# Kernel optimization log

Measured on AMD Instinct MI355X. Metric: run time of the kernel, lower is better.

Reference implementation:

```python
import jax, jax.numpy as jnp
import numpy as np

BATCH, SEQ = 4, 2048
D_MODEL, D_STATE, D_CONV, HEADDIM = 512, 128, 4, 64
D_INNER = 1024          # expand * d_model
NHEADS = 16             # d_inner / headdim
CONV_DIM = D_INNER + 2 * D_STATE   # 1280 (ngroups=1)
D_IN_PROJ = 2 * D_INNER + 2 * D_STATE + NHEADS  # 2320


def setup_inputs() -> dict:
    key = jax.random.key(0)
    ks = jax.random.split(key, 7)
    x = jax.random.normal(ks[0], (BATCH, SEQ, D_MODEL), jnp.float32)
    norm_weight = jnp.ones((D_MODEL,), jnp.float32)
    in_proj_w = jax.random.normal(ks[1], (D_IN_PROJ, D_MODEL), jnp.float32) * 0.02
    conv_w = jax.random.normal(ks[2], (CONV_DIM, 1, D_CONV), jnp.float32) * 0.2
    conv_b = jnp.zeros((CONV_DIM,), jnp.float32)
    dt_bias = jax.random.normal(ks[3], (NHEADS,), jnp.float32) * 0.1
    A_log = jnp.log(jax.random.uniform(ks[4], (NHEADS,), jnp.float32, 1.0, 16.0))
    D_param = jnp.ones((NHEADS,), jnp.float32)
    gated_norm_weight = jnp.ones((D_INNER,), jnp.float32)
    out_proj_w = jax.random.normal(ks[5], (D_MODEL, D_INNER), jnp.float32) * 0.02
    return dict(x=x, norm_weight=norm_weight, in_proj_w=in_proj_w, conv_w=conv_w,
                conv_b=conv_b, dt_bias=dt_bias, A_log=A_log, D_param=D_param,
                gated_norm_weight=gated_norm_weight, out_proj_w=out_proj_w)


def _rmsnorm(x, w, eps):
    return w * (x * jax.lax.rsqrt(jnp.mean(x * x, axis=-1, keepdims=True) + eps))


def _mamba2_forward(x, norm_weight, in_proj_w, conv_w, conv_b, dt_bias,
                    A_log, D_param, gated_norm_weight, out_proj_w):
    b, l, _ = x.shape
    u = _rmsnorm(x, norm_weight, 1e-6)                       # pre-norm (eps=1e-6)
    zxbcdt = u @ in_proj_w.T                                 # (b,l,2320)
    z = zxbcdt[..., :D_INNER]                                # gate
    xBC = zxbcdt[..., D_INNER:D_INNER + CONV_DIM]            # (b,l,1280)
    dt = zxbcdt[..., D_INNER + CONV_DIM:]                    # (b,l,nheads)
    dt = jax.nn.softplus(dt + dt_bias)

    # causal depthwise conv1d over time + SiLU
    conv = jax.lax.conv_general_dilated(
        xBC.transpose(0, 2, 1), conv_w, window_strides=(1,),
        padding=[(D_CONV - 1, 0)], feature_group_count=CONV_DIM,
        dimension_numbers=('NCH', 'OIH', 'NCH'))
    xBC = jax.nn.silu((conv + conv_b[None, :, None]).transpose(0, 2, 1))

    xs = xBC[..., :D_INNER].reshape(b, l, NHEADS, HEADDIM)   # (b,l,h,p)
    Bmat = xBC[..., D_INNER:D_INNER + D_STATE]               # (b,l,n)
    Cmat = xBC[..., D_INNER + D_STATE:]                      # (b,l,n)

    A = -jnp.exp(A_log)                                      # (h,)
    dA = jnp.exp(dt * A)                                     # (b,l,h)
    dtx = dt[..., None] * xs                                 # (b,l,h,p)

    def step(h, inp):
        dA_t, dtx_t, B_t, C_t = inp                          # (b,h),(b,h,p),(b,n),(b,n)
        h = h * dA_t[..., None, None] + dtx_t[..., None] * B_t[:, None, None, :]
        y = jnp.einsum('bhpn,bn->bhp', h, C_t)
        return h, y

    h0 = jnp.zeros((b, NHEADS, HEADDIM, D_STATE), x.dtype)
    _, ys = jax.lax.scan(step, h0, (dA.transpose(1, 0, 2), dtx.transpose(1, 0, 2, 3),
                                    Bmat.transpose(1, 0, 2), Cmat.transpose(1, 0, 2)))
    y = ys.transpose(1, 0, 2, 3) + xs * D_param[None, None, :, None]  # D skip
    y = y.reshape(b, l, D_INNER)

    y = _rmsnorm(y * jax.nn.silu(z), gated_norm_weight, 1e-5)  # RMSNormGated (eps=1e-5)
    return x + y @ out_proj_w.T                                # residual


def reference(x, norm_weight, in_proj_w, conv_w, conv_b, dt_bias,
              A_log, D_param, gated_norm_weight, out_proj_w):
    return _mamba2_forward(x, norm_weight, in_proj_w, conv_w, conv_b, dt_bias,
                           A_log, D_param, gated_norm_weight, out_proj_w)
```

## Files before the change

### kernel.cpp

```cpp
#include <hip/hip_runtime.h>
#include <cstdint>
#include <cstddef>

#define B_ 4
#define L_ 2048
#define DMODEL 512
#define DINNER 1024
#define DSTATE 128
#define NH 16
#define HD 64
#define CONVDIM 1280
#define NPROJ 2320
#define NPAD 2432
#define ML (B_*L_)
#define Q_ 64
#define NCH 32

typedef __bf16 bf16x8 __attribute__((ext_vector_type(8)));
typedef float f32x4 __attribute__((ext_vector_type(4)));
typedef float f32x16 __attribute__((ext_vector_type(16)));

__device__ __forceinline__ float bf2f(ushort u) {
  union { unsigned int i; float f; } v; v.i = ((unsigned int)u) << 16; return v.f;
}
__device__ __forceinline__ ushort f2bf(float f) {
  union { float f; unsigned int i; } v; v.f = f;
  unsigned int u = v.i;
  unsigned int r = (u + 0x7fffu + ((u >> 16) & 1u)) >> 16;
  return (ushort)r;
}
__device__ __forceinline__ float siluf(float x) { return x / (1.f + __expf(-x)); }

__device__ __forceinline__ void gl_lds16(const void* g, void* l) {
  __builtin_amdgcn_global_load_lds(
      (const __attribute__((address_space(1))) unsigned int*)g,
      (__attribute__((address_space(3))) unsigned int*)l,
      16, 0, 0);
}

__global__ __launch_bounds__(256) void k_cvt(const float* __restrict__ wi, const float* __restrict__ wo,
                                             const float* __restrict__ gw,
                                             ushort* __restrict__ oi, ushort* __restrict__ oo) {
  int idx = blockIdx.x * 256 + threadIdx.x;
  const int n1 = NPAD * DMODEL;
  if (idx < n1) {
    int n = idx / DMODEL, k = idx % DMODEL;
    oi[idx] = f2bf((n < NPROJ) ? wi[(size_t)n * DMODEL + k] : 0.f);
  } else {
    int j = idx - n1;
    if (j < DMODEL * DINNER) oo[j] = f2bf(wo[j] * gw[j & (DINNER - 1)]);
  }
}

__global__ __launch_bounds__(256) void k_rmsnorm(const float* __restrict__ x, const float* __restrict__ w,
                                                 ushort* __restrict__ u) {
  int row = blockIdx.x * 4 + (threadIdx.x >> 6);
  int lane = threadIdx.x & 63;
  const float* xr = x + (size_t)row * DMODEL + lane * 8;
  float4 a = *(const float4*)xr;
  float4 b = *(const float4*)(xr + 4);
  float ss = a.x*a.x + a.y*a.y + a.z*a.z + a.w*a.w + b.x*b.x + b.y*b.y + b.z*b.z + b.w*b.w;
  ss += __shfl_xor(ss, 1);  ss += __shfl_xor(ss, 2);  ss += __shfl_xor(ss, 4);
  ss += __shfl_xor(ss, 8);  ss += __shfl_xor(ss, 16); ss += __shfl_xor(ss, 32);
  float sc = rsqrtf(ss * (1.f / DMODEL) + 1e-6f);
  const float* wr = w + lane * 8;
  float4 wa = *(const float4*)wr;
  float4 wb = *(const float4*)(wr + 4);
  union { ushort s[8]; int4 v; } o;
  o.s[0] = f2bf(a.x * wa.x * sc); o.s[1] = f2bf(a.y * wa.y * sc);
  o.s[2] = f2bf(a.z * wa.z * sc); o.s[3] = f2bf(a.w * wa.w * sc);
  o.s[4] = f2bf(b.x * wb.x * sc); o.s[5] = f2bf(b.y * wb.y * sc);
  o.s[6] = f2bf(b.z * wb.z * sc); o.s[7] = f2bf(b.w * wb.w * sc);
  *(int4*)(u + (size_t)row * DMODEL + lane * 8) = o.v;
}

template <int EPI, int BM, int BN, int MR, int NR>
__global__ __launch_bounds__(256) void gemm_bt(const ushort* __restrict__ A, const ushort* __restrict__ Bm,
                                               void* __restrict__ Cout, const float* __restrict__ resid,
                                               const float* __restrict__ rescale,
                                               int M, int N, int K, int gx) {
  constexpr int WM = MR * 32, WN = NR * 32;
  constexpr int WAVES_N = BN / WN;
  constexpr int CH_A = BM / 8, CH_B = BN / 8;
  constexpr int PER_A = CH_A / 4, PER_B = CH_B / 4;
  constexpr int SL = PER_A + PER_B;
  __shared__ __align__(16) ushort lA[2][BM * 64];
  __shared__ __align__(16) ushort lB[2][BN * 64];
  const int nwg = gridDim.x;
  const int cpx = nwg >> 3;
  const int bid = blockIdx.x;
  const int swz = (bid & 7) * cpx + (bid >> 3);
  const int n0 = (swz % gx) * BN, m0 = (swz / gx) * BM;
  const int t = threadIdx.x;
  const int wave = t >> 6, lane = t & 63;
  const int wr = wave / WAVES_N, wc = wave % WAVES_N;
  const int r3 = lane >> 3;
  const int ce = (((lane & 7) ^ r3) << 3);
  const int nt = K >> 6;
  f32x16 acc[MR][NR] = {};
  auto stage = [&](int buf, int k0) {
#pragma unroll
    for (int i = 0; i < PER_A; ++i) {
      int chunk = wave * PER_A + i;
      int row = chunk * 8 + r3;
      gl_lds16(A + (size_t)(m0 + row) * K + k0 + ce, (char*)&lA[buf][0] + chunk * 1024);
    }
#pragma unroll
    for (int i = 0; i < PER_B; ++i) {
      int chunk = wave * PER_B + i;
      int row = chunk * 8 + r3;
      gl_lds16(Bm + (size_t)(n0 + row) * K + k0 + ce, (char*)&lB[buf][0] + chunk * 1024);
    }
  };
  stage(0, 0);
  const int rsel = lane & 31;
  const int khi = (lane >> 5) << 3;
  const int kswz = (lane & 7) << 3;
  for (int kt = 0; kt < nt; ++kt) {
    const int cur = kt & 1;
    if (kt + 1 < nt) {
      stage(cur ^ 1, (kt + 1) << 6);
      if constexpr (SL == 8) asm volatile("s_waitcnt vmcnt(8)" ::: "memory");
      else if constexpr (SL == 6) asm volatile("s_waitcnt vmcnt(6)" ::: "memory");
      else asm volatile("s_waitcnt vmcnt(0)" ::: "memory");
    } else {
      asm volatile("s_waitcnt vmcnt(0)" ::: "memory");
    }
    __builtin_amdgcn_s_barrier();
#pragma unroll
    for (int kk = 0; kk < 64; kk += 16) {
      const int kcol = (kk + khi) ^ kswz;
      bf16x8 af[MR], bfr[NR];
#pragma unroll
      for (int m = 0; m < MR; ++m)
        af[m] = *reinterpret_cast<const bf16x8*>(&lA[cur][(wr * WM + m * 32 + rsel) * 64 + kcol]);
#pragma unroll
      for (int n = 0; n < NR; ++n)
        bfr[n] = *reinterpret_cast<const bf16x8*>(&lB[cur][(wc * WN + n * 32 + rsel) * 64 + kcol]);
#pragma unroll
      for (int m = 0; m < MR; ++m)
#pragma unroll
        for (int n = 0; n < NR; ++n)
          acc[m][n] = __builtin_amdgcn_mfma_f32_32x32x16_bf16(af[m], bfr[n], acc[m][n], 0, 0, 0);
    }
    __builtin_amdgcn_s_barrier();
  }
  const int coln = lane & 31;
  const int rbase = (lane >> 5) << 2;
#pragma unroll
  for (int m = 0; m < MR; ++m) {
#pragma unroll
    for (int n = 0; n < NR; ++n) {
      int gm0 = m0 + wr * WM + m * 32 + rbase;
      int gn = n0 + wc * WN + n * 32 + coln;
#pragma unroll
      for (int r = 0; r < 16; ++r) {
        int gm = gm0 + (r & 3) + 8 * (r >> 2);
        float v = acc[m][n][r];
        if (EPI == 0) {
          ((ushort*)Cout)[(size_t)gm * N + gn] = f2bf(v);
        } else {
          ((float*)Cout)[(size_t)gm * N + gn] = v * rescale[gm] + resid[(size_t)gm * N + gn];
        }
      }
    }
  }
}

__global__ __launch_bounds__(256) void k_dtcum(const ushort* __restrict__ zx, const float* __restrict__ dt_bias,
                                               const float* __restrict__ A_log, float* __restrict__ dtb,
                                               float* __restrict__ acum, float* __restrict__ rs) {
  int flat = blockIdx.x * 256 + threadIdx.x;
  if (flat < ML) rs[flat] = 0.f;
  int gid = blockIdx.x * 4 + (threadIdx.x >> 6);
  int lane = threadIdx.x & 63;
  int c = gid & 31, h = (gid >> 5) & 15, b = gid >> 9;
  int row = b * L_ + c * Q_ + lane;
  float raw = bf2f(zx[(size_t)row * NPAD + DINNER + CONVDIM + h]) + dt_bias[h];
  float dtv = raw > 20.f ? raw : log1pf(expf(raw));
  dtb[(size_t)row * NH + h] = dtv;
  float a = dtv * (-__expf(A_log[h]));
#pragma unroll
  for (int d = 1; d < 64; d <<= 1) {
    float o = __shfl_up(a, d);
    if (lane >= d) a += o;
  }
  acum[(size_t)row * NH + h] = a;
}

__global__ __launch_bounds__(256) void k_conv(const ushort* __restrict__ zx, const float* __restrict__ cw,
                                              const float* __restrict__ cb, ushort* __restrict__ convBC,
                                              ushort* __restrict__ XT, ushort* __restrict__ BT) {
  int t = blockIdx.x * 256 + threadIdx.x;
  int ch = t % CONVDIM;
  int rb = t / CONVDIM;
  int lb = rb & 63, b = rb >> 6;
  int l0 = lb * 32;
  float4 wv = *(const float4*)(cw + ch * 4);
  float bias = cb[ch];
  const size_t rowb = (size_t)b * L_;
  const ushort* ip = zx + (rowb + l0) * NPAD + DINNER + ch;
  float x0 = 0.f, x1 = 0.f, x2 = 0.f;
  if (l0 >= 3) {
    x0 = bf2f(ip[-3 * NPAD]); x1 = bf2f(ip[-2 * NPAD]); x2 = bf2f(ip[-1 * NPAD]);
  }
  ushort* xdst = nullptr; ushort* bdst = nullptr; ushort* bcdst = nullptr;
  if (ch < DINNER) {
    int h = ch >> 6, p = ch & 63;
    xdst = XT + ((size_t)(b * NH + h) * HD + p) * L_ + l0;
  } else if (ch < DINNER + DSTATE) {
    int n = ch - DINNER;
    bdst = BT + ((size_t)b * DSTATE + n) * L_ + l0;
    bcdst = convBC + (rowb + l0) * 256 + n;
  } else {
    int n = ch - DINNER - DSTATE;
    bcdst = convBC + (rowb + l0) * 256 + 128 + n;
  }
  union U8 { int4 v; ushort s[8]; } buf;
#pragma unroll
  for (int i = 0; i < 32; ++i) {
    float x3 = bf2f(ip[(size_t)i * NPAD]);
    float v = wv.x * x0 + wv.y * x1 + wv.z * x2 + wv.w * x3 + bias;
    ushort sv = f2bf(siluf(v));
    x0 = x1; x1 = x2; x2 = x3;
    buf.s[i & 7] = sv;
    if (bcdst) bcdst[(size_t)i * 256] = sv;
    if ((i & 7) == 7) {
      if (xdst) *(int4*)(xdst + (i & ~7)) = buf.v;
      if (bdst) *(int4*)(bdst + (i & ~7)) = buf.v;
    }
  }
}

__global__ __launch_bounds__(256) void k_state(const ushort* __restrict__ XT, const ushort* __restrict__ BT,
                                               const float* __restrict__ dtb, const float* __restrict__ acum,
                                               ushort* __restrict__ Sbuf) {
  __shared__ __align__(16) ushort sXW[64 * 72];
  __shared__ __align__(16) ushort sBT[128 * 64];
  __shared__ float sDt[64], sCum[64], sW[64];
  const int blk = blockIdx.x;
  const int c = blk & 31, h = (blk >> 5) & 15, b = blk >> 9;
  const int row0 = b * L_ + c * Q_;
  const int tid = threadIdx.x;
  const int wave = tid >> 6, lane = tid & 63;
  const int r3 = lane >> 3;
  const int ce = (((lane & 7) ^ r3) << 3);
  const ushort* btb = BT + (size_t)b * DSTATE * L_ + c * Q_;
#pragma unroll
  for (int i = 0; i < 4; ++i) {
    int chunk = wave * 4 + i;
    int row = chunk * 8 + r3;
    gl_lds16(btb + (size_t)row * L_ + ce, (char*)sBT + chunk * 1024);
  }
  if (tid < 64) {
    sDt[tid]  = dtb[(size_t)(row0 + tid) * NH + h];
    sCum[tid] = acum[(size_t)(row0 + tid) * NH + h];
  }
  __syncthreads();
  if (tid < 64) sW[tid] = sDt[tid] * __expf(sCum[63] - sCum[tid]);
  __syncthreads();
  const ushort* xtb = XT + (size_t)(b * NH + h) * HD * L_ + c * Q_;
#pragma unroll
  for (int j = 0; j < 2; ++j) {
    int u = tid * 2 + j;
    int p = u >> 3, t8 = (u & 7) * 8;
    union { int4 v; ushort s[8]; } xv, ov;
    xv.v = *(const int4*)(xtb + (size_t)p * L_ + t8);
    float4 wa = *(const float4*)&sW[t8];
    float4 wb2 = *(const float4*)&sW[t8 + 4];
    ov.s[0] = f2bf(bf2f(xv.s[0]) * wa.x); ov.s[1] = f2bf(bf2f(xv.s[1]) * wa.y);
    ov.s[2] = f2bf(bf2f(xv.s[2]) * wa.z); ov.s[3] = f2bf(bf2f(xv.s[3]) * wa.w);
    ov.s[4] = f2bf(bf2f(xv.s[4]) * wb2.x); ov.s[5] = f2bf(bf2f(xv.s[5]) * wb2.y);
    ov.s[6] = f2bf(bf2f(xv.s[6]) * wb2.z); ov.s[7] = f2bf(bf2f(xv.s[7]) * wb2.w);
    *(int4*)&sXW[p * 72 + t8] = ov.v;
  }
  asm volatile("s_waitcnt vmcnt(0)" ::: "memory");
  __syncthreads();
  const int rsel = lane & 31;
  const int khi = (lane >> 5) << 3;
  const int kswz = (lane & 7) << 3;
  f32x16 acc[2] = {};
#pragma unroll
  for (int kk = 0; kk < 64; kk += 16) {
    const int kA = kk + khi;
    const int kB = kA ^ kswz;
    bf16x8 bfrg = *(const bf16x8*)&sBT[(wave * 32 + rsel) * 64 + kB];
#pragma unroll
    for (int m = 0; m < 2; ++m) {
      bf16x8 afrg = *(const bf16x8*)&sXW[(m * 32 + rsel) * 72 + kA];
      acc[m] = __builtin_amdgcn_mfma_f32_32x32x16_bf16(afrg, bfrg, acc[m], 0, 0, 0);
    }
  }
  ushort* Sp = Sbuf + (size_t)((b * NH + h) * NCH + c) * (HD * DSTATE);
  const int ncol = wave * 32 + (lane & 31);
  const int rbase = (lane >> 5) << 2;
#pragma unroll
  for (int m = 0; m < 2; ++m)
#pragma unroll
    for (int r = 0; r < 16; ++r) {
      int prow = m * 32 + rbase + (r & 3) + 8 * (r >> 2);
      Sp[prow * DSTATE + ncol] = f2bf(acc[m][r]);
    }
}

__global__ __launch_bounds__(256) void k_scan2(ushort* __restrict__ Sbuf, const float* __restrict__ acum) {
  const int blk = blockIdx.x;
  const int ps = blk & 3, bh = blk >> 2;
  const int b = bh >> 4, h = bh & 15;
  const int off = ps * 2048 + threadIdx.x * 8;
  ushort* base = Sbuf + (size_t)bh * NCH * (HD * DSTATE) + off;
  float alphas[NCH];
#pragma unroll
  for (int c = 0; c < NCH; ++c)
    alphas[c] = __expf(acum[(size_t)(b * L_ + c * Q_ + 63) * NH + h]);
  union U8 { int4 v; ushort s[8]; };
  U8 pf[4];
#pragma unroll
  for (int i = 0; i < 4; ++i) pf[i].v = *(const int4*)(base + (size_t)i * (HD * DSTATE));
  float hreg[8] = {};
  U8 hv;
#pragma unroll
  for (int c = 0; c < NCH; ++c) {
    U8 cur = pf[c & 3];
    if (c + 4 < NCH) pf[c & 3].v = *(const int4*)(base + (size_t)(c + 4) * (HD * DSTATE));
#pragma unroll
    for (int i = 0; i < 8; ++i) hv.s[i] = f2bf(hreg[i]);
    *(int4*)(base + (size_t)c * (HD * DSTATE)) = hv.v;
#pragma unroll
    for (int i = 0; i < 8; ++i) hreg[i] = fmaf(alphas[c], hreg[i], bf2f(cur.s[i]));
  }
}

__global__ __launch_bounds__(256) void k_y(const ushort* __restrict__ convBC, const ushort* __restrict__ XT,
                                           const ushort* __restrict__ zx, const ushort* __restrict__ Hin,
                                           const float* __restrict__ dtb, const float* __restrict__ acum,
                                           const float* __restrict__ Dp, ushort* __restrict__ yb,
                                           float* __restrict__ rs) {
  __shared__ __align__(16) ushort sC[64 * 136];
  __shared__ __align__(16) ushort sB[64 * 136];
  __shared__ __align__(16) ushort sH[64 * 136];
  __shared__ __align__(16) ushort sXS[64 * 64];
  __shared__ float sDt[64], sCum[64];
  const int blk = blockIdx.x;
  const int c = blk & 31, h = (blk >> 5) & 15, b = blk >> 9;
  const int row0 = b * L_ + c * Q_;
  const int tid = threadIdx.x;
  const int wave = tid >> 6, lane = tid & 63;
  const int r3 = lane >> 3;
  const int ce = (((lane & 7) ^ r3) << 3);
  const ushort* xtb = XT + (size_t)(b * NH + h) * HD * L_ + c * Q_;
#pragma unroll
  for (int i = 0; i < 2; ++i) {
    int chunk = wave * 2 + i;
    int row = chunk * 8 + r3;
    gl_lds16(xtb + (size_t)row * L_ + ce, (char*)sXS + chunk * 1024);
  }
  if (tid < 64) {
    sDt[tid]  = dtb[(size_t)(row0 + tid) * NH + h];
    sCum[tid] = acum[(size_t)(row0 + tid) * NH + h];
  }
  const ushort* Hp = Hin + (size_t)((b * NH + h) * NCH + c) * (HD * DSTATE);
#pragma unroll
  for (int i = 0; i < 4; ++i) {
    int idx = i * 256 + tid;
    int r = idx >> 4, n8 = (idx & 15) * 8;
    const ushort* src = convBC + (size_t)(row0 + r) * 256 + n8;
    *(int4*)&sB[r * 136 + n8] = *(const int4*)src;
    *(int4*)&sC[r * 136 + n8] = *(const int4*)(src + 128);
    *(int4*)&sH[r * 136 + n8] = *(const int4*)(Hp + (size_t)r * DSTATE + n8);
  }
  asm volatile("s_waitcnt vmcnt(0)" ::: "memory");
  __syncthreads();
  const int rsel = lane & 15;
  const int t0 = wave * 16;
  const int kswz = (lane & 7) << 3;
  f32x4 g[4] = {};
  f32x4 y2[4] = {};
#pragma unroll
  for (int k0 = 0; k0 < 128; k0 += 32) {
    int ksel = k0 + ((lane >> 4) << 3);
    bf16x8 af = *(const bf16x8*)&sC[(t0 + rsel) * 136 + ksel];
#pragma unroll
    for (int s = 0; s < 4; ++s) {
      bf16x8 bf_ = *(const bf16x8*)&sB[(s * 16 + rsel) * 136 + ksel];
      g[s] = __builtin_amdgcn_mfma_f32_16x16x32_bf16(af, bf_, g[s], 0, 0, 0);
      bf16x8 hf = *(const bf16x8*)&sH[(s * 16 + rsel) * 136 + ksel];
      y2[s] = __builtin_amdgcn_mfma_f32_16x16x32_bf16(af, hf, y2[s], 0, 0, 0);
    }
  }
  {
    int trow = t0 + ((lane >> 4) << 2);
#pragma unroll
    for (int s = 0; s < 4; ++s) {
      int sc_ = s * 16 + (lane & 15);
      float dts = sDt[sc_], cums = sCum[sc_];
#pragma unroll
      for (int r = 0; r < 4; ++r) {
        int t2 = trow + r;
        float mv = (sc_ <= t2) ? g[s][r] * dts * __expf(sCum[t2] - cums) : 0.f;
        sC[t2 * 136 + sc_] = f2bf(mv);
      }
    }
  }
  f32x4 yi[4] = {};
#pragma unroll
  for (int k0 = 0; k0 < 64; k0 += 32) {
    int ksel = k0 + ((lane >> 4) << 3);
    bf16x8 af = *(const bf16x8*)&sC[(t0 + rsel) * 136 + ksel];
#pragma unroll
    for (int p = 0; p < 4; ++p) {
      bf16x8 bf_ = *(const bf16x8*)&sXS[(p * 16 + rsel) * 64 + (ksel ^ kswz)];
      yi[p] = __builtin_amdgcn_mfma_f32_16x16x32_bf16(af, bf_, yi[p], 0, 0, 0);
    }
  }
  const float Dh = Dp[h];
  int trow = t0 + ((lane >> 4) << 2);
  float rsum[4] = {0.f, 0.f, 0.f, 0.f};
#pragma unroll
  for (int p = 0; p < 4; ++p) {
    int pc = p * 16 + (lane & 15);
#pragma unroll
    for (int r = 0; r < 4; ++r) {
      int t2 = trow + r;
      float xval = bf2f(sXS[pc * 64 + (t2 ^ ((pc & 7) << 3))]);
      float v = yi[p][r] + __expf(sCum[t2]) * y2[p][r] + Dh * xval;
      float zf = bf2f(zx[(size_t)(row0 + t2) * NPAD + h * HD + pc]);
      float gg = v * siluf(zf);
      rsum[r] += gg * gg;
      yb[(size_t)(row0 + t2) * DINNER + h * HD + pc] = f2bf(gg);
    }
  }
#pragma unroll
  for (int r = 0; r < 4; ++r) {
    float s = rsum[r];
    s += __shfl_xor(s, 1); s += __shfl_xor(s, 2); s += __shfl_xor(s, 4); s += __shfl_xor(s, 8);
    if ((lane & 15) == 0) atomicAdd(&rs[row0 + trow + r], s);
  }
}

__global__ __launch_bounds__(256) void k_scale(float* __restrict__ rs) {
  int i = blockIdx.x * 256 + threadIdx.x;
  rs[i] = rsqrtf(rs[i] * (1.f / DINNER) + 1e-5f);
}

extern "C" void kernel_launch(void* const* d_in, const int* in_sizes, int n_in,
                              void* d_out, int out_size, void* d_ws, size_t ws_size,
                              hipStream_t stream) {
  const float* x         = (const float*)d_in[0];
  const float* norm_w    = (const float*)d_in[1];
  const float* in_proj_w = (const float*)d_in[2];
  const float* conv_w    = (const float*)d_in[3];
  const float* conv_b    = (const float*)d_in[4];
  const float* dt_bias   = (const float*)d_in[5];
  const float* A_log     = (const float*)d_in[6];
  const float* D_param   = (const float*)d_in[7];
  const float* gnw       = (const float*)d_in[8];
  const float* out_proj_w= (const float*)d_in[9];

  char* ws = (char*)d_ws;
  ushort* u      = (ushort*)(ws + 0);
  ushort* convBC = (ushort*)(ws + 0);
  ushort* BT     = (ushort*)(ws + 4194304);
  float*  rs     = (float*)(ws + 6291456);
  ushort* Wb     = (ushort*)(ws + 8388608);
  ushort* Woutb  = (ushort*)(ws + 10878976);
  float*  dtb    = (float*)(ws + 11927552);
  float*  acum   = (float*)(ws + 12451840);
  ushort* zx     = (ushort*)(ws + 12976128);
  ushort* XT     = (ushort*)(ws + 52822016);
  ushort* yb     = (ushort*)(ws + 69599232);
  ushort* Sbuf   = (ushort*)(ws + 86376448);

  k_cvt<<<(NPAD * DMODEL + DMODEL * DINNER + 255) / 256, 256, 0, stream>>>(in_proj_w, out_proj_w, gnw, Wb, Woutb);
  k_rmsnorm<<<ML / 4, 256, 0, stream>>>(x, norm_w, u);
  gemm_bt<0, 128, 128, 2, 2><<<(NPAD / 128) * (ML / 128), 256, 0, stream>>>(u, Wb, (void*)zx, nullptr, nullptr, ML, NPAD, DMODEL, NPAD / 128);
  k_dtcum<<<512, 256, 0, stream>>>(zx, dt_bias, A_log, dtb, acum, rs);
  k_conv<<<CONVDIM, 256, 0, stream>>>(zx, conv_w, conv_b, convBC, XT, BT);
  k_state<<<2048, 256, 0, stream>>>(XT, BT, dtb, acum, Sbuf);
  k_scan2<<<256, 256, 0, stream>>>(Sbuf, acum);
  k_y<<<2048, 256, 0, stream>>>(convBC, XT, zx, Sbuf, dtb, acum, D_param, yb, rs);
  k_scale<<<ML / 256, 256, 0, stream>>>(rs);
  gemm_bt<3, 128, 64, 2, 1><<<(DMODEL / 64) * (ML / 128), 256, 0, stream>>>(yb, Woutb, d_out, x, rs, ML, DMODEL, DINNER, DMODEL / 64);
}
```

Baseline: 146.5 us.

## Merge prep and conv/dt kernels, fold rms scale into GEMM, XOR-swizzle LDS loads

Merges weight conversion with the input RMSNorm, and the dt cumsum with the causal conv, into single launches. Drops the separate k_scale kernel by computing the rsqrt inside the out-projection epilogue. Stores convBC and the chunk states in an XOR-swizzled layout so k_y can fetch them with direct global-to-LDS loads into unpadded, conflict-free shared buffers. Also adds a separate small buffer for the decay mask. This cuts launch overhead and the cost of staging through registers, but the swizzle must match in every producer and consumer, and the epilogue now does redundant rsqrt work.

```diff
diff --git a/kernel.cpp b/kernel.cpp
--- a/kernel.cpp
+++ b/kernel.cpp
@@ -38,23 +38,26 @@
       16, 0, 0);
 }
 
-__global__ __launch_bounds__(256) void k_cvt(const float* __restrict__ wi, const float* __restrict__ wo,
-                                             const float* __restrict__ gw,
-                                             ushort* __restrict__ oi, ushort* __restrict__ oo) {
-  int idx = blockIdx.x * 256 + threadIdx.x;
-  const int n1 = NPAD * DMODEL;
-  if (idx < n1) {
-    int n = idx / DMODEL, k = idx % DMODEL;
-    oi[idx] = f2bf((n < NPROJ) ? wi[(size_t)n * DMODEL + k] : 0.f);
-  } else {
-    int j = idx - n1;
-    if (j < DMODEL * DINNER) oo[j] = f2bf(wo[j] * gw[j & (DINNER - 1)]);
-  }
-}
-
-__global__ __launch_bounds__(256) void k_rmsnorm(const float* __restrict__ x, const float* __restrict__ w,
-                                                 ushort* __restrict__ u) {
-  int row = blockIdx.x * 4 + (threadIdx.x >> 6);
+__global__ __launch_bounds__(256) void k_prep(const float* __restrict__ wi, const float* __restrict__ wo,
+                                              const float* __restrict__ gw, const float* __restrict__ x,
+                                              const float* __restrict__ nw,
+                                              ushort* __restrict__ oi, ushort* __restrict__ oo,
+                                              ushort* __restrict__ u) {
+  const int CVT_BLKS = (NPAD * DMODEL + DMODEL * DINNER) / 256;
+  int bid = blockIdx.x;
+  if (bid < CVT_BLKS) {
+    int idx = bid * 256 + threadIdx.x;
+    const int n1 = NPAD * DMODEL;
+    if (idx < n1) {
+      int n = idx / DMODEL, k = idx % DMODEL;
+      oi[idx] = f2bf((n < NPROJ) ? wi[(size_t)n * DMODEL + k] : 0.f);
+    } else {
+      int j = idx - n1;
+      oo[j] = f2bf(wo[j] * gw[j & (DINNER - 1)]);
+    }
+    return;
+  }
+  int row = (bid - CVT_BLKS) * 4 + (threadIdx.x >> 6);
   int lane = threadIdx.x & 63;
   const float* xr = x + (size_t)row * DMODEL + lane * 8;
   float4 a = *(const float4*)xr;
@@ -63,7 +66,7 @@
   ss += __shfl_xor(ss, 1);  ss += __shfl_xor(ss, 2);  ss += __shfl_xor(ss, 4);
   ss += __shfl_xor(ss, 8);  ss += __shfl_xor(ss, 16); ss += __shfl_xor(ss, 32);
   float sc = rsqrtf(ss * (1.f / DMODEL) + 1e-6f);
-  const float* wr = w + lane * 8;
+  const float* wr = nw + lane * 8;
   float4 wa = *(const float4*)wr;
   float4 wb = *(const float4*)(wr + 4);
   union { ushort s[8]; int4 v; } o;
@@ -77,7 +80,7 @@
 template <int EPI, int BM, int BN, int MR, int NR>
 __global__ __launch_bounds__(256) void gemm_bt(const ushort* __restrict__ A, const ushort* __restrict__ Bm,
                                                void* __restrict__ Cout, const float* __restrict__ resid,
-                                               const float* __restrict__ rescale,
+                                               const float* __restrict__ rs,
                                                int M, int N, int K, int gx) {
   constexpr int WM = MR * 32, WN = NR * 32;
   constexpr int WAVES_N = BN / WN;
@@ -160,38 +163,42 @@
         if (EPI == 0) {
           ((ushort*)Cout)[(size_t)gm * N + gn] = f2bf(v);
         } else {
-          ((float*)Cout)[(size_t)gm * N + gn] = v * rescale[gm] + resid[(size_t)gm * N + gn];
+          float sc_ = rsqrtf(rs[gm] * (1.f / DINNER) + 1e-5f);
+          ((float*)Cout)[(size_t)gm * N + gn] = v * sc_ + resid[(size_t)gm * N + gn];
         }
       }
     }
   }
 }
 
-__global__ __launch_bounds__(256) void k_dtcum(const ushort* __restrict__ zx, const float* __restrict__ dt_bias,
-                                               const float* __restrict__ A_log, float* __restrict__ dtb,
-                                               float* __restrict__ acum, float* __restrict__ rs) {
-  int flat = blockIdx.x * 256 + threadIdx.x;
-  if (flat < ML) rs[flat] = 0.f;
-  int gid = blockIdx.x * 4 + (threadIdx.x >> 6);
-  int lane = threadIdx.x & 63;
-  int c = gid & 31, h = (gid >> 5) & 15, b = gid >> 9;
-  int row = b * L_ + c * Q_ + lane;
-  float raw = bf2f(zx[(size_t)row * NPAD + DINNER + CONVDIM + h]) + dt_bias[h];
-  float dtv = raw > 20.f ? raw : log1pf(expf(raw));
-  dtb[(size_t)row * NH + h] = dtv;
-  float a = dtv * (-__expf(A_log[h]));
-#pragma unroll
-  for (int d = 1; d < 64; d <<= 1) {
-    float o = __shfl_up(a, d);
-    if (lane >= d) a += o;
-  }
-  acum[(size_t)row * NH + h] = a;
-}
-
-__global__ __launch_bounds__(256) void k_conv(const ushort* __restrict__ zx, const float* __restrict__ cw,
-                                              const float* __restrict__ cb, ushort* __restrict__ convBC,
-                                              ushort* __restrict__ XT, ushort* __restrict__ BT) {
-  int t = blockIdx.x * 256 + threadIdx.x;
+__global__ __launch_bounds__(256) void k_convdt(const ushort* __restrict__ zx, const float* __restrict__ cw,
+                                                const float* __restrict__ cb, const float* __restrict__ dt_bias,
+                                                const float* __restrict__ A_log,
+                                                ushort* __restrict__ convBC, ushort* __restrict__ XT,
+                                                ushort* __restrict__ BT,
+                                                float* __restrict__ dtb, float* __restrict__ acum,
+                                                float* __restrict__ rs) {
+  int bid = blockIdx.x;
+  if (bid >= CONVDIM) {
+    int flat = (bid - CONVDIM) * 256 + threadIdx.x;
+    if (flat < ML) rs[flat] = 0.f;
+    int gid = (bid - CONVDIM) * 4 + (threadIdx.x >> 6);
+    int lane = threadIdx.x & 63;
+    int c = gid & 31, h = (gid >> 5) & 15, b = gid >> 9;
+    int row = b * L_ + c * Q_ + lane;
+    float raw = bf2f(zx[(size_t)row * NPAD + DINNER + CONVDIM + h]) + dt_bias[h];
+    float dtv = raw > 20.f ? raw : log1pf(expf(raw));
+    dtb[(size_t)row * NH + h] = dtv;
+    float a = dtv * (-__expf(A_log[h]));
+#pragma unroll
+    for (int d = 1; d < 64; d <<= 1) {
+      float o = __shfl_up(a, d);
+      if (lane >= d) a += o;
+    }
+    acum[(size_t)row * NH + h] = a;
+    return;
+  }
+  int t = bid * 256 + threadIdx.x;
   int ch = t % CONVDIM;
   int rb = t / CONVDIM;
   int lb = rb & 63, b = rb >> 6;
@@ -204,17 +211,18 @@
   if (l0 >= 3) {
     x0 = bf2f(ip[-3 * NPAD]); x1 = bf2f(ip[-2 * NPAD]); x2 = bf2f(ip[-1 * NPAD]);
   }
-  ushort* xdst = nullptr; ushort* bdst = nullptr; ushort* bcdst = nullptr;
+  ushort* xdst = nullptr; ushort* bdst = nullptr;
+  ushort* bcb2 = nullptr; int col0 = 0;
   if (ch < DINNER) {
     int h = ch >> 6, p = ch & 63;
     xdst = XT + ((size_t)(b * NH + h) * HD + p) * L_ + l0;
   } else if (ch < DINNER + DSTATE) {
     int n = ch - DINNER;
     bdst = BT + ((size_t)b * DSTATE + n) * L_ + l0;
-    bcdst = convBC + (rowb + l0) * 256 + n;
+    bcb2 = convBC + (rowb + l0) * 256; col0 = n;
   } else {
     int n = ch - DINNER - DSTATE;
-    bcdst = convBC + (rowb + l0) * 256 + 128 + n;
+    bcb2 = convBC + (rowb + l0) * 256; col0 = 128 + n;
   }
   union U8 { int4 v; ushort s[8]; } buf;
 #pragma unroll
@@ -224,7 +232,7 @@
     ushort sv = f2bf(siluf(v));
     x0 = x1; x1 = x2; x2 = x3;
     buf.s[i & 7] = sv;
-    if (bcdst) bcdst[(size_t)i * 256] = sv;
+    if (bcb2) bcb2[(size_t)i * 256 + (col0 ^ ((i & 7) << 3))] = sv;
     if ((i & 7) == 7) {
       if (xdst) *(int4*)(xdst + (i & ~7)) = buf.v;
       if (bdst) *(int4*)(bdst + (i & ~7)) = buf.v;
@@ -299,7 +307,7 @@
 #pragma unroll
     for (int r = 0; r < 16; ++r) {
       int prow = m * 32 + rbase + (r & 3) + 8 * (r >> 2);
-      Sp[prow * DSTATE + ncol] = f2bf(acc[m][r]);
+      Sp[prow * DSTATE + (ncol ^ ((prow & 7) << 3))] = f2bf(acc[m][r]);
     }
 }
 
@@ -336,9 +344,9 @@
                                            const float* __restrict__ dtb, const float* __restrict__ acum,
                                            const float* __restrict__ Dp, ushort* __restrict__ yb,
                                            float* __restrict__ rs) {
-  __shared__ __align__(16) ushort sC[64 * 136];
-  __shared__ __align__(16) ushort sB[64 * 136];
-  __shared__ __align__(16) ushort sH[64 * 136];
+  __shared__ __align__(16) ushort sBC[64 * 256];
+  __shared__ __align__(16) ushort sH[64 * 128];
+  __shared__ __align__(16) ushort sM[64 * 72];
   __shared__ __align__(16) ushort sXS[64 * 64];
   __shared__ float sDt[64], sCum[64];
   const int blk = blockIdx.x;
@@ -348,6 +356,18 @@
   const int wave = tid >> 6, lane = tid & 63;
   const int r3 = lane >> 3;
   const int ce = (((lane & 7) ^ r3) << 3);
+  const char* bcb = (const char*)(convBC + (size_t)row0 * 256);
+#pragma unroll
+  for (int i = 0; i < 8; ++i) {
+    int chunk = wave * 8 + i;
+    gl_lds16(bcb + chunk * 1024 + lane * 16, (char*)sBC + chunk * 1024);
+  }
+  const char* Hp = (const char*)(Hin + (size_t)((b * NH + h) * NCH + c) * (HD * DSTATE));
+#pragma unroll
+  for (int i = 0; i < 4; ++i) {
+    int chunk = wave * 4 + i;
+    gl_lds16(Hp + chunk * 1024 + lane * 16, (char*)sH + chunk * 1024);
+  }
   const ushort* xtb = XT + (size_t)(b * NH + h) * HD * L_ + c * Q_;
 #pragma unroll
   for (int i = 0; i < 2; ++i) {
@@ -359,32 +379,23 @@
     sDt[tid]  = dtb[(size_t)(row0 + tid) * NH + h];
     sCum[tid] = acum[(size_t)(row0 + tid) * NH + h];
   }
-  const ushort* Hp = Hin + (size_t)((b * NH + h) * NCH + c) * (HD * DSTATE);
-#pragma unroll
-  for (int i = 0; i < 4; ++i) {
-    int idx = i * 256 + tid;
-    int r = idx >> 4, n8 = (idx & 15) * 8;
-    const ushort* src = convBC + (size_t)(row0 + r) * 256 + n8;
-    *(int4*)&sB[r * 136 + n8] = *(const int4*)src;
-    *(int4*)&sC[r * 136 + n8] = *(const int4*)(src + 128);
-    *(int4*)&sH[r * 136 + n8] = *(const int4*)(Hp + (size_t)r * DSTATE + n8);
-  }
   asm volatile("s_waitcnt vmcnt(0)" ::: "memory");
   __syncthreads();
   const int rsel = lane & 15;
   const int t0 = wave * 16;
-  const int kswz = (lane & 7) << 3;
+  const int rk = (rsel & 7) << 3;
   f32x4 g[4] = {};
   f32x4 y2[4] = {};
 #pragma unroll
   for (int k0 = 0; k0 < 128; k0 += 32) {
     int ksel = k0 + ((lane >> 4) << 3);
-    bf16x8 af = *(const bf16x8*)&sC[(t0 + rsel) * 136 + ksel];
+    int kx = ksel ^ rk;
+    bf16x8 af = *(const bf16x8*)&sBC[(t0 + rsel) * 256 + 128 + kx];
 #pragma unroll
     for (int s = 0; s < 4; ++s) {
-      bf16x8 bf_ = *(const bf16x8*)&sB[(s * 16 + rsel) * 136 + ksel];
+      bf16x8 bf_ = *(const bf16x8*)&sBC[(s * 16 + rsel) * 256 + kx];
       g[s] = __builtin_amdgcn_mfma_f32_16x16x32_bf16(af, bf_, g[s], 0, 0, 0);
-      bf16x8 hf = *(const bf16x8*)&sH[(s * 16 + rsel) * 136 + ksel];
+      bf16x8 hf = *(const bf16x8*)&sH[(s * 16 + rsel) * 128 + kx];
       y2[s] = __builtin_amdgcn_mfma_f32_16x16x32_bf16(af, hf, y2[s], 0, 0, 0);
     }
   }
@@ -398,7 +409,7 @@
       for (int r = 0; r < 4; ++r) {
         int t2 = trow + r;
         float mv = (sc_ <= t2) ? g[s][r] * dts * __expf(sCum[t2] - cums) : 0.f;
-        sC[t2 * 136 + sc_] = f2bf(mv);
+        sM[t2 * 72 + sc_] = f2bf(mv);
       }
     }
   }
@@ -406,10 +417,10 @@
 #pragma unroll
   for (int k0 = 0; k0 < 64; k0 += 32) {
     int ksel = k0 + ((lane >> 4) << 3);
-    bf16x8 af = *(const bf16x8*)&sC[(t0 + rsel) * 136 + ksel];
+    bf16x8 af = *(const bf16x8*)&sM[(t0 + rsel) * 72 + ksel];
 #pragma unroll
     for (int p = 0; p < 4; ++p) {
-      bf16x8 bf_ = *(const bf16x8*)&sXS[(p * 16 + rsel) * 64 + (ksel ^ kswz)];
+      bf16x8 bf_ = *(const bf16x8*)&sXS[(p * 16 + rsel) * 64 + (ksel ^ rk)];
       yi[p] = __builtin_amdgcn_mfma_f32_16x16x32_bf16(af, bf_, yi[p], 0, 0, 0);
     }
   }
@@ -436,11 +447,6 @@
     s += __shfl_xor(s, 1); s += __shfl_xor(s, 2); s += __shfl_xor(s, 4); s += __shfl_xor(s, 8);
     if ((lane & 15) == 0) atomicAdd(&rs[row0 + trow + r], s);
   }
-}
-
-__global__ __launch_bounds__(256) void k_scale(float* __restrict__ rs) {
-  int i = blockIdx.x * 256 + threadIdx.x;
-  rs[i] = rsqrtf(rs[i] * (1.f / DINNER) + 1e-5f);
 }
 
 extern "C" void kernel_launch(void* const* d_in, const int* in_sizes, int n_in,
@@ -471,14 +477,12 @@
   ushort* yb     = (ushort*)(ws + 69599232);
   ushort* Sbuf   = (ushort*)(ws + 86376448);
 
-  k_cvt<<<(NPAD * DMODEL + DMODEL * DINNER + 255) / 256, 256, 0, stream>>>(in_proj_w, out_proj_w, gnw, Wb, Woutb);
-  k_rmsnorm<<<ML / 4, 256, 0, stream>>>(x, norm_w, u);
+  const int CVT_BLKS = (NPAD * DMODEL + DMODEL * DINNER) / 256;
+  k_prep<<<CVT_BLKS + ML / 4, 256, 0, stream>>>(in_proj_w, out_proj_w, gnw, x, norm_w, Wb, Woutb, u);
   gemm_bt<0, 128, 128, 2, 2><<<(NPAD / 128) * (ML / 128), 256, 0, stream>>>(u, Wb, (void*)zx, nullptr, nullptr, ML, NPAD, DMODEL, NPAD / 128);
-  k_dtcum<<<512, 256, 0, stream>>>(zx, dt_bias, A_log, dtb, acum, rs);
-  k_conv<<<CONVDIM, 256, 0, stream>>>(zx, conv_w, conv_b, convBC, XT, BT);
+  k_convdt<<<CONVDIM + 512, 256, 0, stream>>>(zx, conv_w, conv_b, dt_bias, A_log, convBC, XT, BT, dtb, acum, rs);
   k_state<<<2048, 256, 0, stream>>>(XT, BT, dtb, acum, Sbuf);
   k_scan2<<<256, 256, 0, stream>>>(Sbuf, acum);
   k_y<<<2048, 256, 0, stream>>>(convBC, XT, zx, Sbuf, dtb, acum, D_param, yb, rs);
-  k_scale<<<ML / 256, 256, 0, stream>>>(rs);
   gemm_bt<3, 128, 64, 2, 1><<<(DMODEL / 64) * (ML / 128), 256, 0, stream>>>(yb, Woutb, d_out, x, rs, ML, DMODEL, DINNER, DMODEL / 64);
 }
```

Measured after the change: 138.4 us. -5.5%, faster.
